# Optimization experiments

Measured on AMD Instinct MI355X. Metric: run time of the kernel, lower is better.

Reference implementation:

```python
import jax, jax.numpy as jnp
import numpy as np

WS = 8            # window size (square)
N = WS * WS       # tokens per window = 64
DIM = 192
HEADS = 6
HDIM = DIM // HEADS
SCALE = HDIM ** -0.5


def _rel_pos_index(ws=WS):
    coords = np.stack(np.meshgrid(np.arange(ws), np.arange(ws), indexing='ij'))  # [2,ws,ws]
    cf = coords.reshape(2, -1)                       # [2, N]
    rc = (cf[:, :, None] - cf[:, None, :]).transpose(1, 2, 0).astype(np.int64)  # [N,N,2]
    rc[:, :, 0] += ws - 1
    rc[:, :, 1] += ws - 1
    rc[:, :, 0] *= 2 * ws - 1
    return jnp.asarray(rc.sum(-1))                   # [N, N]

REL_IDX = _rel_pos_index()


def _linear(x, w, b=None):
    y = jnp.einsum('...i,oi->...o', x, w)
    return y if b is None else y + b


def _diff_attn(q_t, k_t, v_t, q_r, k_r, v_r, bias, lam):
    # q,k,v: [B, H, N, d]; bias: [H, N, N]; lam scalar
    at = jax.nn.softmax(jnp.einsum('bhqd,bhkd->bhqk', q_t * SCALE, k_t) + bias, axis=-1)
    ar = jax.nn.softmax(jnp.einsum('bhqd,bhkd->bhqk', q_r * SCALE, k_r) + bias, axis=-1)
    dt = at - lam * ar
    dr = ar - lam * at
    ot = jnp.einsum('bhqk,bhkd->bhqd', dt, v_t)
    orf = jnp.einsum('bhqk,bhkd->bhqd', dr, v_r)
    return ot, orf


def _heads(x, B):
    # [B, N, C] -> [B, H, N, d]
    return x.reshape(B, N, HEADS, HDIM).transpose(0, 2, 1, 3)


def _unheads(x, B):
    return x.transpose(0, 2, 1, 3).reshape(B, N, DIM)


def setup_inputs() -> dict:
    key = jax.random.key(0)
    ks = jax.random.split(key, 16)
    nW = 1024
    p = lambda k, shp: (jax.random.normal(k, shp, jnp.float32) * 0.02)
    return {
        'x_windows': jax.random.normal(ks[0], (nW, N, DIM), jnp.float32),
        'y_windows': jax.random.normal(ks[1], (nW, N, DIM), jnp.float32),
        'sa_qkv_w': p(ks[2], (3 * DIM, DIM)), 'sa_qkv_b': jnp.zeros((3 * DIM,), jnp.float32),
        'sa_ct_w': p(ks[3], (DIM, DIM)), 'sa_cr_w': p(ks[4], (DIM, DIM)),
        'ca_q_w': p(ks[5], (DIM, DIM)), 'ca_q_b': jnp.zeros((DIM,), jnp.float32),
        'ca_kv_w': p(ks[6], (2 * DIM, DIM)), 'ca_kv_b': jnp.zeros((2 * DIM,), jnp.float32),
        'ca_ct_w': p(ks[7], (DIM, DIM)), 'ca_cr_w': p(ks[8], (DIM, DIM)),
        'rpb_table': p(ks[9], ((2 * WS - 1) * (2 * WS - 1), HEADS)),
        'proj_sa_w': p(ks[10], (DIM, DIM)), 'proj_sa_b': jnp.zeros((DIM,), jnp.float32),
        'proj_ca_w': p(ks[11], (DIM, DIM)), 'proj_ca_b': jnp.zeros((DIM,), jnp.float32),
        'lambda_sa': jnp.float32(0.1), 'lambda_ca': jnp.float32(0.1),
        'sa_enh': jnp.float32(0.1), 'ca_enh': jnp.float32(0.1),
    }


def reference(x_windows, y_windows, sa_qkv_w, sa_qkv_b, sa_ct_w, sa_cr_w,
              ca_q_w, ca_q_b, ca_kv_w, ca_kv_b, ca_ct_w, ca_cr_w,
              rpb_table, proj_sa_w, proj_sa_b, proj_ca_w, proj_ca_b,
              lambda_sa, lambda_ca, sa_enh, ca_enh):
    B = x_windows.shape[0]
    bias = rpb_table[REL_IDX.reshape(-1)].reshape(N, N, HEADS).transpose(2, 0, 1)  # [H,N,N]

    # ---- Self-attention branch (batch-dim concat) ----
    t_enh = x_windows + sa_enh * _linear(y_windows, sa_cr_w)
    r_enh = y_windows + sa_enh * _linear(x_windows, sa_ct_w)
    qkv_t = _linear(t_enh, sa_qkv_w, sa_qkv_b).reshape(B, N, 3, HEADS, HDIM).transpose(2, 0, 3, 1, 4)
    qkv_r = _linear(r_enh, sa_qkv_w, sa_qkv_b).reshape(B, N, 3, HEADS, HDIM).transpose(2, 0, 3, 1, 4)
    lam_sa = jnp.clip(jax.nn.sigmoid(lambda_sa), 0.01, 0.99)
    ot, orf = _diff_attn(qkv_t[0], qkv_t[1], qkv_t[2], qkv_r[0], qkv_r[1], qkv_r[2], bias, lam_sa)
    sa_t = _linear(_unheads(ot, B), proj_sa_w, proj_sa_b)
    sa_r = _linear(_unheads(orf, B), proj_sa_w, proj_sa_b)
    sa_out = jnp.concatenate([sa_t, sa_r], axis=0)  # [2B, N, C]

    # ---- Cross-attention branch (seq-dim concat) ----
    t_enh = x_windows + ca_enh * _linear(y_windows, ca_cr_w)
    r_enh = y_windows + ca_enh * _linear(x_windows, ca_ct_w)
    q_t = _heads(_linear(t_enh, ca_q_w, ca_q_b), B)
    q_r = _heads(_linear(r_enh, ca_q_w, ca_q_b), B)
    xcat = jnp.concatenate([t_enh, r_enh], axis=1)  # [B, 2N, C]
    kv = _linear(xcat, ca_kv_w, ca_kv_b).reshape(B, 2 * N, 2, HEADS, HDIM).transpose(2, 0, 3, 1, 4)
    k, v = kv[0], kv[1]
    k_t, k_r = k[:, :, :N], k[:, :, N:]
    v_t, v_r = v[:, :, :N], v[:, :, N:]
    lam_ca = jnp.clip(jax.nn.sigmoid(lambda_ca), 0.01, 0.99)
    ot, orf = _diff_attn(q_t, k_t, v_t, q_r, k_r, v_r, bias, lam_ca)
    ca_t = _linear(_unheads(ot, B), proj_ca_w, proj_ca_b)
    ca_r = _linear(_unheads(orf, B), proj_ca_w, proj_ca_b)
    ca_out = jnp.concatenate([ca_t, ca_r], axis=1)  # [B, 2N, C]

    # pack into a single array: [4B, N, C]
    return jnp.concatenate([sa_out, ca_out.reshape(2 * B, N, DIM)], axis=0)
```

## Files before the change

kernel.cpp:

```cpp
#include <hip/hip_runtime.h>

#define KD 192
#define H6 6

typedef __attribute__((ext_vector_type(8))) short bf16x8;
typedef __attribute__((ext_vector_type(4))) float f32x4;

__device__ __forceinline__ unsigned short f2bf(float f) {
  unsigned u = __float_as_uint(f);
  u += 0x7FFFu + ((u >> 16) & 1u);
  return (unsigned short)(u >> 16);
}

__global__ void bias_k(const float* __restrict__ tab, float* __restrict__ biasw) {
  int t = blockIdx.x * 256 + threadIdx.x;
  if (t >= H6 * 64 * 64) return;
  int h = t >> 12, rem = t & 4095, i = rem >> 6, j = rem & 63;
  int idx = ((i >> 3) - (j >> 3) + 7) * 15 + ((i & 7) - (j & 7) + 7);
  biasw[t] = tab[idx * H6 + h];
}

__global__ void convert_k(
    const float* __restrict__ sa_qkv_w, const float* __restrict__ sa_ct_w,
    const float* __restrict__ sa_cr_w, const float* __restrict__ ca_q_w,
    const float* __restrict__ ca_kv_w, const float* __restrict__ ca_ct_w,
    const float* __restrict__ ca_cr_w, const float* __restrict__ proj_sa_w,
    const float* __restrict__ proj_ca_w,
    const float* __restrict__ ca_q_b, const float* __restrict__ ca_kv_b,
    unsigned short* __restrict__ wqkv, unsigned short* __restrict__ wct_sa,
    unsigned short* __restrict__ wcr_sa, unsigned short* __restrict__ wca,
    unsigned short* __restrict__ wct_ca, unsigned short* __restrict__ wcr_ca,
    unsigned short* __restrict__ wpsa, unsigned short* __restrict__ wpca,
    float* __restrict__ bca)
{
  int t = blockIdx.x * 256 + threadIdx.x;
  if (t < 110592) {
    int i = t << 2;
    const float* s; unsigned short* d;
    if (i < 110592)      { s = sa_qkv_w + i;            d = wqkv + i; }
    else if (i < 147456) { s = sa_ct_w + (i - 110592);  d = wct_sa + (i - 110592); }
    else if (i < 184320) { s = sa_cr_w + (i - 147456);  d = wcr_sa + (i - 147456); }
    else if (i < 221184) { s = ca_q_w + (i - 184320);   d = wca + (i - 184320); }
    else if (i < 294912) { s = ca_kv_w + (i - 221184);  d = wca + 36864 + (i - 221184); }
    else if (i < 331776) { s = ca_ct_w + (i - 294912);  d = wct_ca + (i - 294912); }
    else if (i < 368640) { s = ca_cr_w + (i - 331776);  d = wcr_ca + (i - 331776); }
    else if (i < 405504) { s = proj_sa_w + (i - 368640); d = wpsa + (i - 368640); }
    else                 { s = proj_ca_w + (i - 405504); d = wpca + (i - 405504); }
    float4 v = *(const float4*)s;
    ushort4 p;
    p.x = f2bf(v.x); p.y = f2bf(v.y); p.z = f2bf(v.z); p.w = f2bf(v.w);
    *(ushort4*)d = p;
  } else if (t < 110592 + 144) {
    int i = (t - 110592) << 2;
    const float* s = (i < 192) ? (ca_q_b + i) : (ca_kv_b + (i - 192));
    *(float4*)(bca + i) = *(const float4*)s;
  }
}

struct FQArgs {
  const unsigned short* Wc[4];
  const unsigned short* Wq[4];
  const float* bias[4];
  unsigned short* dq[4];
  unsigned short* dk[4];
  unsigned short* dv[4];
};

__global__ __launch_bounds__(256) void fqkv_k(
    const float* __restrict__ x, const float* __restrict__ y,
    const float* __restrict__ sap, const float* __restrict__ cap,
    FQArgs args, float SC)
{
  __shared__ short Al[64][200], Wl[64][200], El[64][200];
  const int tid = threadIdx.x;
  const int mblk = blockIdx.x, z = blockIdx.y;
  const int row = tid >> 2, cb = (tid & 3) * 48;
  const float* A    = (z & 1) ? x : y;
  const float* resd = (z & 1) ? y : x;
  const float sc = (z < 2) ? *sap : *cap;

  {
    const float* ap = A + ((long)mblk * 64 + row) * KD + cb;
#pragma unroll
    for (int j = 0; j < 12; ++j) {
      float4 v = *(const float4*)(ap + 4 * j);
      ushort4 p;
      p.x = f2bf(v.x); p.y = f2bf(v.y); p.z = f2bf(v.z); p.w = f2bf(v.w);
      *(ushort4*)&Al[row][cb + 4 * j] = p;
    }
  }
  const int lane = tid & 63, wv = tid >> 6;
  const int qn = lane & 15, g = lane >> 4;
  const int mloc = 16 * wv + 4 * g;
  const f32x4 zero = {0.f, 0.f, 0.f, 0.f};

  for (int ct = 0; ct < 3; ++ct) {
    {
      const unsigned short* Wp = args.Wc[z] + ((long)ct * 64 + row) * KD + cb;
#pragma unroll
      for (int j = 0; j < 6; ++j)
        *(float4*)&Wl[row][cb + 8 * j] = *(const float4*)(Wp + 8 * j);
    }
    __syncthreads();
    f32x4 acc[4];
#pragma unroll
    for (int nt = 0; nt < 4; ++nt) acc[nt] = zero;
#pragma unroll
    for (int ks = 0; ks < 6; ++ks) {
      bf16x8 a = *(const bf16x8*)&Al[16 * wv + qn][32 * ks + 8 * g];
#pragma unroll
      for (int nt = 0; nt < 4; ++nt) {
        bf16x8 bfr = *(const bf16x8*)&Wl[16 * nt + qn][32 * ks + 8 * g];
        acc[nt] = __builtin_amdgcn_mfma_f32_16x16x32_bf16(a, bfr, acc[nt], 0, 0, 0);
      }
    }
#pragma unroll
    for (int nt = 0; nt < 4; ++nt) {
      const int c = ct * 64 + 16 * nt + qn;
#pragma unroll
      for (int r = 0; r < 4; ++r)
        El[mloc + r][c] =
            f2bf(resd[((long)mblk * 64 + mloc + r) * KD + c] + sc * acc[nt][r]);
    }
    __syncthreads();
  }

  for (int wt = 0; wt < 9; ++wt) {
    {
      const unsigned short* Wp = args.Wq[z] + ((long)wt * 64 + row) * KD + cb;
#pragma unroll
      for (int j = 0; j < 6; ++j)
        *(float4*)&Wl[row][cb + 8 * j] = *(const float4*)(Wp + 8 * j);
    }
    __syncthreads();
    f32x4 acc[4];
#pragma unroll
    for (int nt = 0; nt < 4; ++nt) acc[nt] = zero;
#pragma unroll
    for (int ks = 0; ks < 6; ++ks) {
      bf16x8 a = *(const bf16x8*)&El[16 * wv + qn][32 * ks + 8 * g];
#pragma unroll
      for (int nt = 0; nt < 4; ++nt) {
        bf16x8 bfr = *(const bf16x8*)&Wl[16 * nt + qn][32 * ks + 8 * g];
        acc[nt] = __builtin_amdgcn_mfma_f32_16x16x32_bf16(a, bfr, acc[nt], 0, 0, 0);
      }
    }
#pragma unroll
    for (int nt = 0; nt < 4; ++nt) {
      const int cg = wt * 64 + 16 * nt + qn;
      const int idx = (cg >= 384) ? 2 : ((cg >= 192) ? 1 : 0);
      const int cc = cg - idx * KD;
      const int h = cc >> 5, d = cc & 31;
      const float bv = args.bias[z][cg];
      const float sca = (idx == 0) ? SC : 1.f;
      const long bwh = (long)mblk * H6 + h;
      if (idx < 2) {
        unsigned short* dst = idx ? args.dk[z] : args.dq[z];
#pragma unroll
        for (int r = 0; r < 4; ++r)
          dst[(bwh * 64 + (mloc + r)) * 32 + d] = f2bf((acc[nt][r] + bv) * sca);
      } else {
        ushort4 p;
        p.x = f2bf(acc[nt][0] + bv);
        p.y = f2bf(acc[nt][1] + bv);
        p.z = f2bf(acc[nt][2] + bv);
        p.w = f2bf(acc[nt][3] + bv);
        *(ushort4*)&args.dv[z][(bwh * 32 + d) * 64 + mloc] = p;
      }
    }
    __syncthreads();
  }
}

struct ProjArgs {
  const unsigned short* A[4];
  const unsigned short* W[4];
  const float* bias[4];
  float* o[4];
  long wstride[4];
};

__global__ __launch_bounds__(256) void proj_k(ProjArgs args)
{
  __shared__ short Al[64][200], Wl[64][200];
  const int tid = threadIdx.x;
  const int mblk = blockIdx.x, z = blockIdx.y;
  const int row = tid >> 2, cb = (tid & 3) * 48;
  {
    const unsigned short* A = args.A[z] + ((long)mblk * 64 + row) * KD + cb;
#pragma unroll
    for (int j = 0; j < 6; ++j)
      *(float4*)&Al[row][cb + 8 * j] = *(const float4*)(A + 8 * j);
  }
  const int lane = tid & 63, wv = tid >> 6;
  const int qn = lane & 15, g = lane >> 4;
  const int mloc = 16 * wv + 4 * g;
  const f32x4 zero = {0.f, 0.f, 0.f, 0.f};
  float* fo = args.o[z] + (long)mblk * args.wstride[z];

  for (int ct = 0; ct < 3; ++ct) {
    {
      const unsigned short* Wp = args.W[z] + ((long)ct * 64 + row) * KD + cb;
#pragma unroll
      for (int j = 0; j < 6; ++j)
        *(float4*)&Wl[row][cb + 8 * j] = *(const float4*)(Wp + 8 * j);
    }
    __syncthreads();
    f32x4 acc[4];
#pragma unroll
    for (int nt = 0; nt < 4; ++nt) acc[nt] = zero;
#pragma unroll
    for (int ks = 0; ks < 6; ++ks) {
      bf16x8 a = *(const bf16x8*)&Al[16 * wv + qn][32 * ks + 8 * g];
#pragma unroll
      for (int nt = 0; nt < 4; ++nt) {
        bf16x8 bfr = *(const bf16x8*)&Wl[16 * nt + qn][32 * ks + 8 * g];
        acc[nt] = __builtin_amdgcn_mfma_f32_16x16x32_bf16(a, bfr, acc[nt], 0, 0, 0);
      }
    }
#pragma unroll
    for (int nt = 0; nt < 4; ++nt) {
      const int c = ct * 64 + 16 * nt + qn;
      const float bv = args.bias[z][c];
#pragma unroll
      for (int r = 0; r < 4; ++r)
        fo[(long)(mloc + r) * KD + c] = acc[nt][r] + bv;
    }
    __syncthreads();
  }
}

__device__ __forceinline__ void softmax_rows2(f32x4 (&S)[4][2]) {
#pragma unroll
  for (int nt = 0; nt < 2; ++nt) {
    float mx = -3.0e38f;
#pragma unroll
    for (int mt = 0; mt < 4; ++mt)
#pragma unroll
      for (int r = 0; r < 4; ++r) mx = fmaxf(mx, S[mt][nt][r]);
    mx = fmaxf(mx, __shfl_xor(mx, 16));
    mx = fmaxf(mx, __shfl_xor(mx, 32));
    float sm = 0.f;
#pragma unroll
    for (int mt = 0; mt < 4; ++mt)
#pragma unroll
      for (int r = 0; r < 4; ++r) {
        float p = __expf(S[mt][nt][r] - mx);
        S[mt][nt][r] = p;
        sm += p;
      }
    sm += __shfl_xor(sm, 16);
    sm += __shfl_xor(sm, 32);
    const float inv = 1.f / sm;
#pragma unroll
    for (int mt = 0; mt < 4; ++mt)
#pragma unroll
      for (int r = 0; r < 4; ++r) S[mt][nt][r] *= inv;
  }
}

__device__ __forceinline__ void diff_attn32(
    const unsigned short* __restrict__ qb, const unsigned short* __restrict__ kb,
    const unsigned short* __restrict__ vTb, long pstride,
    const float* __restrict__ bh, float lam,
    unsigned short* __restrict__ o_t, unsigned short* __restrict__ o_r,
    long base, int b, int h, int qoff, int qn, int g,
    short (*Pl)[32][72])
{
  f32x4 st[4][2], sr[4][2];
#pragma unroll
  for (int mt = 0; mt < 4; ++mt)
#pragma unroll
    for (int nt = 0; nt < 2; ++nt) {
      f32x4 bv = *(const f32x4*)&bh[(qoff + 16 * nt + qn) * 64 + 16 * mt + 4 * g];
      st[mt][nt] = bv;
      sr[mt][nt] = bv;
    }
  {
    bf16x8 ka[4], qv[2];
#pragma unroll
    for (int mt = 0; mt < 4; ++mt)
      ka[mt] = *(const bf16x8*)&kb[base + (16 * mt + qn) * 32 + 8 * g];
#pragma unroll
    for (int nt = 0; nt < 2; ++nt)
      qv[nt] = *(const bf16x8*)&qb[base + (qoff + 16 * nt + qn) * 32 + 8 * g];
#pragma unroll
    for (int mt = 0; mt < 4; ++mt)
#pragma unroll
      for (int nt = 0; nt < 2; ++nt)
        st[mt][nt] = __builtin_amdgcn_mfma_f32_16x16x32_bf16(ka[mt], qv[nt], st[mt][nt], 0, 0, 0);
#pragma unroll
    for (int mt = 0; mt < 4; ++mt)
      ka[mt] = *(const bf16x8*)&kb[pstride + base + (16 * mt + qn) * 32 + 8 * g];
#pragma unroll
    for (int nt = 0; nt < 2; ++nt)
      qv[nt] = *(const bf16x8*)&qb[pstride + base + (qoff + 16 * nt + qn) * 32 + 8 * g];
#pragma unroll
    for (int mt = 0; mt < 4; ++mt)
#pragma unroll
      for (int nt = 0; nt < 2; ++nt)
        sr[mt][nt] = __builtin_amdgcn_mfma_f32_16x16x32_bf16(ka[mt], qv[nt], sr[mt][nt], 0, 0, 0);
  }
  softmax_rows2(st);
  softmax_rows2(sr);
#pragma unroll
  for (int mt = 0; mt < 4; ++mt)
#pragma unroll
    for (int nt = 0; nt < 2; ++nt) {
      ushort4 pt, pr;
#pragma unroll
      for (int r = 0; r < 4; ++r) {
        float a = st[mt][nt][r], rr = sr[mt][nt][r];
        ((unsigned short*)&pt)[r] = f2bf(a - lam * rr);
        ((unsigned short*)&pr)[r] = f2bf(rr - lam * a);
      }
      *(ushort4*)&Pl[0][16 * nt + qn][16 * mt + 4 * g] = pt;
      *(ushort4*)&Pl[1][16 * nt + qn][16 * mt + 4 * g] = pr;
    }
  const f32x4 zero = {0.f, 0.f, 0.f, 0.f};
#pragma unroll
  for (int p = 0; p < 2; ++p) {
    const unsigned short* vv = p ? (vTb + pstride) : vTb;
    unsigned short* outp = p ? o_r : o_t;
    f32x4 oa[2][2];
#pragma unroll
    for (int i = 0; i < 2; ++i)
#pragma unroll
      for (int nt = 0; nt < 2; ++nt) oa[i][nt] = zero;
#pragma unroll
    for (int ks = 0; ks < 2; ++ks) {
      bf16x8 va0 = *(const bf16x8*)&vv[base + (0 + qn) * 64 + 32 * ks + 8 * g];
      bf16x8 va1 = *(const bf16x8*)&vv[base + (16 + qn) * 64 + 32 * ks + 8 * g];
#pragma unroll
      for (int nt = 0; nt < 2; ++nt) {
        bf16x8 pb = *(const bf16x8*)&Pl[p][16 * nt + qn][32 * ks + 8 * g];
        oa[0][nt] = __builtin_amdgcn_mfma_f32_16x16x32_bf16(va0, pb, oa[0][nt], 0, 0, 0);
        oa[1][nt] = __builtin_amdgcn_mfma_f32_16x16x32_bf16(va1, pb, oa[1][nt], 0, 0, 0);
      }
    }
#pragma unroll
    for (int d16 = 0; d16 < 2; ++d16)
#pragma unroll
      for (int nt = 0; nt < 2; ++nt) {
        const int q = qoff + 16 * nt + qn;
        ushort4 pk;
        pk.x = f2bf(oa[d16][nt][0]); pk.y = f2bf(oa[d16][nt][1]);
        pk.z = f2bf(oa[d16][nt][2]); pk.w = f2bf(oa[d16][nt][3]);
        *(ushort4*)&outp[((long)b * 64 + q) * KD + h * 32 + 16 * d16 + 4 * g] = pk;
      }
  }
}

__global__ __launch_bounds__(256) void attn_k(
    const unsigned short* __restrict__ saq, const unsigned short* __restrict__ sak,
    const unsigned short* __restrict__ savT,
    const unsigned short* __restrict__ caq, const unsigned short* __restrict__ cak,
    const unsigned short* __restrict__ cavT,
    const float* __restrict__ biasw, const float* __restrict__ lsp,
    const float* __restrict__ lcp,
    unsigned short* __restrict__ o0, unsigned short* __restrict__ o1,
    unsigned short* __restrict__ o2, unsigned short* __restrict__ o3,
    long pstride)
{
  __shared__ short Pl[4][2][32][72];
  const int wv = threadIdx.x >> 6, lane = threadIdx.x & 63;
  const int qn = lane & 15, g = lane >> 4;
  const int qoff = (wv & 1) * 32;
  const int wh = blockIdx.x * 2 + (wv >> 1);
  const int b = wh / H6, h = wh - b * H6;
  const float* bh = biasw + (long)h * 4096;
  const long base = (long)wh * 2048;
  float ls = 1.f / (1.f + __expf(-*lsp));
  ls = fminf(fmaxf(ls, 0.01f), 0.99f);
  float lc = 1.f / (1.f + __expf(-*lcp));
  lc = fminf(fmaxf(lc, 0.01f), 0.99f);
  diff_attn32(saq, sak, savT, pstride, bh, ls, o0, o1, base, b, h, qoff, qn, g, Pl[wv]);
  diff_attn32(caq, cak, cavT, pstride, bh, lc, o2, o3, base, b, h, qoff, qn, g, Pl[wv]);
}

extern "C" void kernel_launch(void* const* d_in, const int* in_sizes, int n_in,
                              void* d_out, int out_size, void* d_ws, size_t ws_size,
                              hipStream_t stream)
{
  const float* x         = (const float*)d_in[0];
  const float* y         = (const float*)d_in[1];
  const float* sa_qkv_w  = (const float*)d_in[2];
  const float* sa_qkv_b  = (const float*)d_in[3];
  const float* sa_ct_w   = (const float*)d_in[4];
  const float* sa_cr_w   = (const float*)d_in[5];
  const float* ca_q_w    = (const float*)d_in[6];
  const float* ca_q_b    = (const float*)d_in[7];
  const float* ca_kv_w   = (const float*)d_in[8];
  const float* ca_kv_b   = (const float*)d_in[9];
  const float* ca_ct_w   = (const float*)d_in[10];
  const float* ca_cr_w   = (const float*)d_in[11];
  const float* rpb       = (const float*)d_in[12];
  const float* proj_sa_w = (const float*)d_in[13];
  const float* proj_sa_b = (const float*)d_in[14];
  const float* proj_ca_w = (const float*)d_in[15];
  const float* proj_ca_b = (const float*)d_in[16];
  const float* lam_sa_p  = (const float*)d_in[17];
  const float* lam_ca_p  = (const float*)d_in[18];
  const float* sa_enh_p  = (const float*)d_in[19];
  const float* ca_enh_p  = (const float*)d_in[20];
  float* out = (float*)d_out;

  const int M = in_sizes[0] / KD;
  const int B = M / 64;
  const long pstride = (long)B * H6 * 2048;

  char* ws = (char*)d_ws;
  float* biasw = (float*)ws;
  float* bca = (float*)(ws + 98304);
  unsigned short* wqkv   = (unsigned short*)(ws + 100864);
  unsigned short* wca    = (unsigned short*)(ws + 322048);
  unsigned short* wct_sa = (unsigned short*)(ws + 543232);
  unsigned short* wcr_sa = (unsigned short*)(ws + 616960);
  unsigned short* wct_ca = (unsigned short*)(ws + 690688);
  unsigned short* wcr_ca = (unsigned short*)(ws + 764416);
  unsigned short* wpsa   = (unsigned short*)(ws + 838144);
  unsigned short* wpca   = (unsigned short*)(ws + 911872);
  long off = 1048576;
  unsigned short* ob0 = (unsigned short*)(ws + off); off += (long)M * KD * 2;
  unsigned short* ob1 = (unsigned short*)(ws + off); off += (long)M * KD * 2;
  unsigned short* ob2 = (unsigned short*)(ws + off); off += (long)M * KD * 2;
  unsigned short* ob3 = (unsigned short*)(ws + off); off += (long)M * KD * 2;
  unsigned short* caq  = (unsigned short*)(ws + off); off += pstride * 4;
  unsigned short* cak  = (unsigned short*)(ws + off); off += pstride * 4;
  unsigned short* cavT = (unsigned short*)(ws + off); off += pstride * 4;
  unsigned short* saq  = (unsigned short*)d_out;
  unsigned short* sak  = saq + 2 * pstride;
  unsigned short* savT = sak + 2 * pstride;

  const float SC = 0.17677669529663687f;

  convert_k<<<dim3(433), dim3(256), 0, stream>>>(
      sa_qkv_w, sa_ct_w, sa_cr_w, ca_q_w, ca_kv_w, ca_ct_w, ca_cr_w,
      proj_sa_w, proj_ca_w, ca_q_b, ca_kv_b,
      wqkv, wct_sa, wcr_sa, wca, wct_ca, wcr_ca, wpsa, wpca, bca);
  bias_k<<<dim3(96), dim3(256), 0, stream>>>(rpb, biasw);

  FQArgs fa;
  fa.Wc[0] = wcr_sa; fa.Wc[1] = wct_sa; fa.Wc[2] = wcr_ca; fa.Wc[3] = wct_ca;
  fa.Wq[0] = wqkv;   fa.Wq[1] = wqkv;   fa.Wq[2] = wca;    fa.Wq[3] = wca;
  fa.bias[0] = sa_qkv_b; fa.bias[1] = sa_qkv_b; fa.bias[2] = bca; fa.bias[3] = bca;
  fa.dq[0] = saq;  fa.dq[1] = saq + pstride;  fa.dq[2] = caq;  fa.dq[3] = caq + pstride;
  fa.dk[0] = sak;  fa.dk[1] = sak + pstride;  fa.dk[2] = cak;  fa.dk[3] = cak + pstride;
  fa.dv[0] = savT; fa.dv[1] = savT + pstride; fa.dv[2] = cavT; fa.dv[3] = cavT + pstride;
  fqkv_k<<<dim3(B, 4), dim3(256), 0, stream>>>(x, y, sa_enh_p, ca_enh_p, fa, SC);

  attn_k<<<dim3(B * H6 / 2), dim3(256), 0, stream>>>(saq, sak, savT, caq, cak, cavT,
                                                     biasw, lam_sa_p, lam_ca_p,
                                                     ob0, ob1, ob2, ob3, pstride);

  ProjArgs pa;
  pa.A[0] = ob0; pa.A[1] = ob1; pa.A[2] = ob2; pa.A[3] = ob3;
  pa.W[0] = wpsa; pa.W[1] = wpsa; pa.W[2] = wpca; pa.W[3] = wpca;
  pa.bias[0] = proj_sa_b; pa.bias[1] = proj_sa_b; pa.bias[2] = proj_ca_b; pa.bias[3] = proj_ca_b;
  pa.o[0] = out;                       pa.wstride[0] = 12288;
  pa.o[1] = out + (long)B * 12288;     pa.wstride[1] = 12288;
  pa.o[2] = out + (long)2 * B * 12288; pa.wstride[2] = 24576;
  pa.o[3] = out + (long)2 * B * 12288 + 12288; pa.wstride[3] = 24576;
  proj_k<<<dim3(B, 4), dim3(256), 0, stream>>>(pa);
}
```

Measured before the change: 665.6 us.

## Restructure fused QKV kernel with register prefetch, 2x2 warp tiling, shared A/E buffer

The fused cross-enhance + QKV projection kernel now prefetches the next 64-row weight tile into registers while MFMAs run on the current tile, so global loads overlap with compute. Warps switch from 16x64 strips to 32x32 quadrant tiles, with A fragments held in registers and reused across weight tiles, which cuts LDS reads. The input and enhanced-activation buffers are merged into one shared array so LDS use drops, and launch bounds request 3 blocks per CU. The cost is higher register pressure from the prefetch registers, A fragments and three sets of accumulators, which could limit occupancy or cause spills.

```diff
diff --git a/kernel.cpp b/kernel.cpp
--- a/kernel.cpp
+++ b/kernel.cpp
@@ -66,12 +66,13 @@
   unsigned short* dv[4];
 };
 
-__global__ __launch_bounds__(256) void fqkv_k(
+__global__ __launch_bounds__(256, 3) void fqkv_k(
     const float* __restrict__ x, const float* __restrict__ y,
     const float* __restrict__ sap, const float* __restrict__ cap,
     FQArgs args, float SC)
 {
-  __shared__ short Al[64][200], Wl[64][200], El[64][200];
+  __shared__ short AE[64][200];
+  __shared__ short Wl[64][200];
   const int tid = threadIdx.x;
   const int mblk = blockIdx.x, z = blockIdx.y;
   const int row = tid >> 2, cb = (tid & 3) * 48;
@@ -79,96 +80,136 @@
   const float* resd = (z & 1) ? y : x;
   const float sc = (z < 2) ? *sap : *cap;
 
+  float4 wpf[6];
   {
     const float* ap = A + ((long)mblk * 64 + row) * KD + cb;
+    const unsigned short* wp = args.Wc[z] + (long)row * KD + cb;
+#pragma unroll
+    for (int j = 0; j < 6; ++j) wpf[j] = *(const float4*)(wp + 8 * j);
 #pragma unroll
     for (int j = 0; j < 12; ++j) {
       float4 v = *(const float4*)(ap + 4 * j);
       ushort4 p;
       p.x = f2bf(v.x); p.y = f2bf(v.y); p.z = f2bf(v.z); p.w = f2bf(v.w);
-      *(ushort4*)&Al[row][cb + 4 * j] = p;
-    }
-  }
+      *(ushort4*)&AE[row][cb + 4 * j] = p;
+    }
+#pragma unroll
+    for (int j = 0; j < 6; ++j) *(float4*)&Wl[row][cb + 8 * j] = wpf[j];
+  }
+  __syncthreads();
+
   const int lane = tid & 63, wv = tid >> 6;
   const int qn = lane & 15, g = lane >> 4;
-  const int mloc = 16 * wv + 4 * g;
+  const int rbase = (wv & 1) * 32, cbase = (wv >> 1) * 32;
   const f32x4 zero = {0.f, 0.f, 0.f, 0.f};
 
-  for (int ct = 0; ct < 3; ++ct) {
+  bf16x8 af[2][6];
+#pragma unroll
+  for (int im = 0; im < 2; ++im)
+#pragma unroll
+    for (int ks = 0; ks < 6; ++ks)
+      af[im][ks] = *(const bf16x8*)&AE[rbase + 16 * im + qn][32 * ks + 8 * g];
+
+  f32x4 acc2[3][2][2];
+#pragma unroll
+  for (int t = 0; t < 3; ++t)
+#pragma unroll
+    for (int im = 0; im < 2; ++im)
+#pragma unroll
+      for (int in = 0; in < 2; ++in) acc2[t][im][in] = zero;
+
+#pragma unroll
+  for (int t = 0; t < 3; ++t) {
     {
-      const unsigned short* Wp = args.Wc[z] + ((long)ct * 64 + row) * KD + cb;
-#pragma unroll
-      for (int j = 0; j < 6; ++j)
-        *(float4*)&Wl[row][cb + 8 * j] = *(const float4*)(Wp + 8 * j);
+      const unsigned short* ns = (t < 2) ? (args.Wc[z] + (long)(t + 1) * 12288)
+                                         : args.Wq[z];
+      const unsigned short* wp = ns + (long)row * KD + cb;
+#pragma unroll
+      for (int j = 0; j < 6; ++j) wpf[j] = *(const float4*)(wp + 8 * j);
+    }
+#pragma unroll
+    for (int ks = 0; ks < 6; ++ks) {
+      bf16x8 wf0 = *(const bf16x8*)&Wl[cbase + qn][32 * ks + 8 * g];
+      bf16x8 wf1 = *(const bf16x8*)&Wl[cbase + 16 + qn][32 * ks + 8 * g];
+      acc2[t][0][0] = __builtin_amdgcn_mfma_f32_16x16x32_bf16(af[0][ks], wf0, acc2[t][0][0], 0, 0, 0);
+      acc2[t][1][0] = __builtin_amdgcn_mfma_f32_16x16x32_bf16(af[1][ks], wf0, acc2[t][1][0], 0, 0, 0);
+      acc2[t][0][1] = __builtin_amdgcn_mfma_f32_16x16x32_bf16(af[0][ks], wf1, acc2[t][0][1], 0, 0, 0);
+      acc2[t][1][1] = __builtin_amdgcn_mfma_f32_16x16x32_bf16(af[1][ks], wf1, acc2[t][1][1], 0, 0, 0);
     }
     __syncthreads();
-    f32x4 acc[4];
-#pragma unroll
-    for (int nt = 0; nt < 4; ++nt) acc[nt] = zero;
+#pragma unroll
+    for (int j = 0; j < 6; ++j) *(float4*)&Wl[row][cb + 8 * j] = wpf[j];
+    __syncthreads();
+  }
+
+#pragma unroll
+  for (int ct = 0; ct < 3; ++ct)
+#pragma unroll
+    for (int im = 0; im < 2; ++im)
+#pragma unroll
+      for (int in = 0; in < 2; ++in) {
+        const int c = ct * 64 + cbase + 16 * in + qn;
+        const int rl = rbase + 16 * im + 4 * g;
+#pragma unroll
+        for (int r = 0; r < 4; ++r)
+          AE[rl + r][c] = f2bf(resd[((long)mblk * 64 + rl + r) * KD + c] +
+                               sc * acc2[ct][im][in][r]);
+      }
+  __syncthreads();
+#pragma unroll
+  for (int im = 0; im < 2; ++im)
+#pragma unroll
+    for (int ks = 0; ks < 6; ++ks)
+      af[im][ks] = *(const bf16x8*)&AE[rbase + 16 * im + qn][32 * ks + 8 * g];
+
+  for (int wt = 0; wt < 9; ++wt) {
+    if (wt < 8) {
+      const unsigned short* wp = args.Wq[z] + (long)(wt + 1) * 12288 + (long)row * KD + cb;
+#pragma unroll
+      for (int j = 0; j < 6; ++j) wpf[j] = *(const float4*)(wp + 8 * j);
+    }
+    f32x4 acc[2][2] = {{zero, zero}, {zero, zero}};
 #pragma unroll
     for (int ks = 0; ks < 6; ++ks) {
-      bf16x8 a = *(const bf16x8*)&Al[16 * wv + qn][32 * ks + 8 * g];
-#pragma unroll
-      for (int nt = 0; nt < 4; ++nt) {
-        bf16x8 bfr = *(const bf16x8*)&Wl[16 * nt + qn][32 * ks + 8 * g];
-        acc[nt] = __builtin_amdgcn_mfma_f32_16x16x32_bf16(a, bfr, acc[nt], 0, 0, 0);
-      }
-    }
-#pragma unroll
-    for (int nt = 0; nt < 4; ++nt) {
-      const int c = ct * 64 + 16 * nt + qn;
-#pragma unroll
-      for (int r = 0; r < 4; ++r)
-        El[mloc + r][c] =
-            f2bf(resd[((long)mblk * 64 + mloc + r) * KD + c] + sc * acc[nt][r]);
-    }
-    __syncthreads();
-  }
-
-  for (int wt = 0; wt < 9; ++wt) {
-    {
-      const unsigned short* Wp = args.Wq[z] + ((long)wt * 64 + row) * KD + cb;
-#pragma unroll
-      for (int j = 0; j < 6; ++j)
-        *(float4*)&Wl[row][cb + 8 * j] = *(const float4*)(Wp + 8 * j);
-    }
-    __syncthreads();
-    f32x4 acc[4];
-#pragma unroll
-    for (int nt = 0; nt < 4; ++nt) acc[nt] = zero;
-#pragma unroll
-    for (int ks = 0; ks < 6; ++ks) {
-      bf16x8 a = *(const bf16x8*)&El[16 * wv + qn][32 * ks + 8 * g];
-#pragma unroll
-      for (int nt = 0; nt < 4; ++nt) {
-        bf16x8 bfr = *(const bf16x8*)&Wl[16 * nt + qn][32 * ks + 8 * g];
-        acc[nt] = __builtin_amdgcn_mfma_f32_16x16x32_bf16(a, bfr, acc[nt], 0, 0, 0);
-      }
-    }
-#pragma unroll
-    for (int nt = 0; nt < 4; ++nt) {
-      const int cg = wt * 64 + 16 * nt + qn;
-      const int idx = (cg >= 384) ? 2 : ((cg >= 192) ? 1 : 0);
-      const int cc = cg - idx * KD;
-      const int h = cc >> 5, d = cc & 31;
-      const float bv = args.bias[z][cg];
-      const float sca = (idx == 0) ? SC : 1.f;
-      const long bwh = (long)mblk * H6 + h;
-      if (idx < 2) {
-        unsigned short* dst = idx ? args.dk[z] : args.dq[z];
-#pragma unroll
-        for (int r = 0; r < 4; ++r)
-          dst[(bwh * 64 + (mloc + r)) * 32 + d] = f2bf((acc[nt][r] + bv) * sca);
-      } else {
-        ushort4 p;
-        p.x = f2bf(acc[nt][0] + bv);
-        p.y = f2bf(acc[nt][1] + bv);
-        p.z = f2bf(acc[nt][2] + bv);
-        p.w = f2bf(acc[nt][3] + bv);
-        *(ushort4*)&args.dv[z][(bwh * 32 + d) * 64 + mloc] = p;
-      }
-    }
-    __syncthreads();
+      bf16x8 wf0 = *(const bf16x8*)&Wl[cbase + qn][32 * ks + 8 * g];
+      bf16x8 wf1 = *(const bf16x8*)&Wl[cbase + 16 + qn][32 * ks + 8 * g];
+      acc[0][0] = __builtin_amdgcn_mfma_f32_16x16x32_bf16(af[0][ks], wf0, acc[0][0], 0, 0, 0);
+      acc[1][0] = __builtin_amdgcn_mfma_f32_16x16x32_bf16(af[1][ks], wf0, acc[1][0], 0, 0, 0);
+      acc[0][1] = __builtin_amdgcn_mfma_f32_16x16x32_bf16(af[0][ks], wf1, acc[0][1], 0, 0, 0);
+      acc[1][1] = __builtin_amdgcn_mfma_f32_16x16x32_bf16(af[1][ks], wf1, acc[1][1], 0, 0, 0);
+    }
+#pragma unroll
+    for (int im = 0; im < 2; ++im)
+#pragma unroll
+      for (int in = 0; in < 2; ++in) {
+        const int cg = wt * 64 + cbase + 16 * in + qn;
+        const int idx = (cg >= 384) ? 2 : ((cg >= 192) ? 1 : 0);
+        const int cc = cg - idx * KD;
+        const int h = cc >> 5, d = cc & 31;
+        const float bv = args.bias[z][cg];
+        const long bwh = (long)mblk * H6 + h;
+        const int rl = rbase + 16 * im + 4 * g;
+        if (idx < 2) {
+          const float sca = idx ? 1.f : SC;
+          unsigned short* dst = idx ? args.dk[z] : args.dq[z];
+#pragma unroll
+          for (int r = 0; r < 4; ++r)
+            dst[(bwh * 64 + rl + r) * 32 + d] = f2bf((acc[im][in][r] + bv) * sca);
+        } else {
+          ushort4 p;
+          p.x = f2bf(acc[im][in][0] + bv);
+          p.y = f2bf(acc[im][in][1] + bv);
+          p.z = f2bf(acc[im][in][2] + bv);
+          p.w = f2bf(acc[im][in][3] + bv);
+          *(ushort4*)&args.dv[z][(bwh * 32 + d) * 64 + rl] = p;
+        }
+      }
+    if (wt < 8) {
+      __syncthreads();
+#pragma unroll
+      for (int j = 0; j < 6; ++j) *(float4*)&Wl[row][cb + 8 * j] = wpf[j];
+      __syncthreads();
+    }
   }
 }
 
```

New measurement: 865.0 us. 29.9% more time.

## Fuse differential attention with output projection in one per-window kernel

Applied to the files above, without the earlier changes.

Adds a fattn_k kernel with one block per window and branch, using 12 waves (one per head and query half). Each block computes both differential attention outputs into shared memory as bf16, then applies the output projection with bias straight into the final buffer. This removes the attention output round trip through global memory and one kernel launch. It needs a larger workspace to hold all q/k/v tensors, so the old three-kernel path is kept as a fallback when the workspace is too small. The 768-thread blocks use a lot of LDS, which may limit occupancy.

```diff
diff --git a/kernel.cpp b/kernel.cpp
--- a/kernel.cpp
+++ b/kernel.cpp
@@ -172,64 +172,6 @@
   }
 }
 
-struct ProjArgs {
-  const unsigned short* A[4];
-  const unsigned short* W[4];
-  const float* bias[4];
-  float* o[4];
-  long wstride[4];
-};
-
-__global__ __launch_bounds__(256) void proj_k(ProjArgs args)
-{
-  __shared__ short Al[64][200], Wl[64][200];
-  const int tid = threadIdx.x;
-  const int mblk = blockIdx.x, z = blockIdx.y;
-  const int row = tid >> 2, cb = (tid & 3) * 48;
-  {
-    const unsigned short* A = args.A[z] + ((long)mblk * 64 + row) * KD + cb;
-#pragma unroll
-    for (int j = 0; j < 6; ++j)
-      *(float4*)&Al[row][cb + 8 * j] = *(const float4*)(A + 8 * j);
-  }
-  const int lane = tid & 63, wv = tid >> 6;
-  const int qn = lane & 15, g = lane >> 4;
-  const int mloc = 16 * wv + 4 * g;
-  const f32x4 zero = {0.f, 0.f, 0.f, 0.f};
-  float* fo = args.o[z] + (long)mblk * args.wstride[z];
-
-  for (int ct = 0; ct < 3; ++ct) {
-    {
-      const unsigned short* Wp = args.W[z] + ((long)ct * 64 + row) * KD + cb;
-#pragma unroll
-      for (int j = 0; j < 6; ++j)
-        *(float4*)&Wl[row][cb + 8 * j] = *(const float4*)(Wp + 8 * j);
-    }
-    __syncthreads();
-    f32x4 acc[4];
-#pragma unroll
-    for (int nt = 0; nt < 4; ++nt) acc[nt] = zero;
-#pragma unroll
-    for (int ks = 0; ks < 6; ++ks) {
-      bf16x8 a = *(const bf16x8*)&Al[16 * wv + qn][32 * ks + 8 * g];
-#pragma unroll
-      for (int nt = 0; nt < 4; ++nt) {
-        bf16x8 bfr = *(const bf16x8*)&Wl[16 * nt + qn][32 * ks + 8 * g];
-        acc[nt] = __builtin_amdgcn_mfma_f32_16x16x32_bf16(a, bfr, acc[nt], 0, 0, 0);
-      }
-    }
-#pragma unroll
-    for (int nt = 0; nt < 4; ++nt) {
-      const int c = ct * 64 + 16 * nt + qn;
-      const float bv = args.bias[z][c];
-#pragma unroll
-      for (int r = 0; r < 4; ++r)
-        fo[(long)(mloc + r) * KD + c] = acc[nt][r] + bv;
-    }
-    __syncthreads();
-  }
-}
-
 __device__ __forceinline__ void softmax_rows2(f32x4 (&S)[4][2]) {
 #pragma unroll
   for (int nt = 0; nt < 2; ++nt) {
@@ -256,6 +198,157 @@
     for (int mt = 0; mt < 4; ++mt)
 #pragma unroll
       for (int r = 0; r < 4; ++r) S[mt][nt][r] *= inv;
+  }
+}
+
+struct FAArgs {
+  const unsigned short* q[2];
+  const unsigned short* k[2];
+  const unsigned short* vT[2];
+  const float* lamp[2];
+  const unsigned short* w[2];
+  const float* pb[2];
+  float* ot[2];
+  float* orr[2];
+  long ostride[2];
+};
+
+__global__ __launch_bounds__(768, 3) void fattn_k(
+    FAArgs args, const float* __restrict__ biasw, long pstride)
+{
+  __shared__ short Ol[2][64][200];
+  __shared__ short Pl[12][32][72];
+  const int tid = threadIdx.x;
+  const int wv = tid >> 6, lane = tid & 63;
+  const int qn = lane & 15, g = lane >> 4;
+  const int b = blockIdx.x, z = blockIdx.y;
+  const int h = wv >> 1, qoff = (wv & 1) * 32;
+  const long base = ((long)b * H6 + h) * 2048;
+  const unsigned short* qb = args.q[z];
+  const unsigned short* kb = args.k[z];
+  const unsigned short* vTb = args.vT[z];
+  float lam = 1.f / (1.f + __expf(-*args.lamp[z]));
+  lam = fminf(fmaxf(lam, 0.01f), 0.99f);
+  const float* bh = biasw + (long)h * 4096;
+  short (*pl)[72] = Pl[wv];
+  const f32x4 zero = {0.f, 0.f, 0.f, 0.f};
+
+  f32x4 st[4][2], sr[4][2];
+#pragma unroll
+  for (int mt = 0; mt < 4; ++mt)
+#pragma unroll
+    for (int nt = 0; nt < 2; ++nt) {
+      f32x4 bv = *(const f32x4*)&bh[(qoff + 16 * nt + qn) * 64 + 16 * mt + 4 * g];
+      st[mt][nt] = bv;
+      sr[mt][nt] = bv;
+    }
+  {
+    bf16x8 ka[4], qv[2];
+#pragma unroll
+    for (int mt = 0; mt < 4; ++mt)
+      ka[mt] = *(const bf16x8*)&kb[base + (16 * mt + qn) * 32 + 8 * g];
+#pragma unroll
+    for (int nt = 0; nt < 2; ++nt)
+      qv[nt] = *(const bf16x8*)&qb[base + (qoff + 16 * nt + qn) * 32 + 8 * g];
+#pragma unroll
+    for (int mt = 0; mt < 4; ++mt)
+#pragma unroll
+      for (int nt = 0; nt < 2; ++nt)
+        st[mt][nt] = __builtin_amdgcn_mfma_f32_16x16x32_bf16(ka[mt], qv[nt], st[mt][nt], 0, 0, 0);
+#pragma unroll
+    for (int mt = 0; mt < 4; ++mt)
+      ka[mt] = *(const bf16x8*)&kb[pstride + base + (16 * mt + qn) * 32 + 8 * g];
+#pragma unroll
+    for (int nt = 0; nt < 2; ++nt)
+      qv[nt] = *(const bf16x8*)&qb[pstride + base + (qoff + 16 * nt + qn) * 32 + 8 * g];
+#pragma unroll
+    for (int mt = 0; mt < 4; ++mt)
+#pragma unroll
+      for (int nt = 0; nt < 2; ++nt)
+        sr[mt][nt] = __builtin_amdgcn_mfma_f32_16x16x32_bf16(ka[mt], qv[nt], sr[mt][nt], 0, 0, 0);
+  }
+  softmax_rows2(st);
+  softmax_rows2(sr);
+#pragma unroll
+  for (int mt = 0; mt < 4; ++mt)
+#pragma unroll
+    for (int nt = 0; nt < 2; ++nt)
+#pragma unroll
+      for (int r = 0; r < 4; ++r) {
+        float a = st[mt][nt][r], rr = sr[mt][nt][r];
+        st[mt][nt][r] = a - lam * rr;
+        sr[mt][nt][r] = rr - lam * a;
+      }
+
+#pragma unroll
+  for (int p = 0; p < 2; ++p) {
+    auto& P = p ? sr : st;
+#pragma unroll
+    for (int mt = 0; mt < 4; ++mt)
+#pragma unroll
+      for (int nt = 0; nt < 2; ++nt) {
+        ushort4 pk;
+        pk.x = f2bf(P[mt][nt][0]); pk.y = f2bf(P[mt][nt][1]);
+        pk.z = f2bf(P[mt][nt][2]); pk.w = f2bf(P[mt][nt][3]);
+        *(ushort4*)&pl[16 * nt + qn][16 * mt + 4 * g] = pk;
+      }
+    const unsigned short* vv = p ? (vTb + pstride) : vTb;
+    f32x4 oa[2][2];
+#pragma unroll
+    for (int i = 0; i < 2; ++i)
+#pragma unroll
+      for (int nt = 0; nt < 2; ++nt) oa[i][nt] = zero;
+#pragma unroll
+    for (int ks = 0; ks < 2; ++ks) {
+      bf16x8 va0 = *(const bf16x8*)&vv[base + (0 + qn) * 64 + 32 * ks + 8 * g];
+      bf16x8 va1 = *(const bf16x8*)&vv[base + (16 + qn) * 64 + 32 * ks + 8 * g];
+#pragma unroll
+      for (int nt = 0; nt < 2; ++nt) {
+        bf16x8 pb8 = *(const bf16x8*)&pl[16 * nt + qn][32 * ks + 8 * g];
+        oa[0][nt] = __builtin_amdgcn_mfma_f32_16x16x32_bf16(va0, pb8, oa[0][nt], 0, 0, 0);
+        oa[1][nt] = __builtin_amdgcn_mfma_f32_16x16x32_bf16(va1, pb8, oa[1][nt], 0, 0, 0);
+      }
+    }
+#pragma unroll
+    for (int d16 = 0; d16 < 2; ++d16)
+#pragma unroll
+      for (int nt = 0; nt < 2; ++nt) {
+        ushort4 pk;
+        pk.x = f2bf(oa[d16][nt][0]); pk.y = f2bf(oa[d16][nt][1]);
+        pk.z = f2bf(oa[d16][nt][2]); pk.w = f2bf(oa[d16][nt][3]);
+        *(ushort4*)&Ol[p][qoff + 16 * nt + qn][h * 32 + 16 * d16 + 4 * g] = pk;
+      }
+  }
+
+  const int cstrip = wv * 16;
+  const unsigned short* wz = args.w[z];
+  bf16x8 wf[6];
+#pragma unroll
+  for (int ks = 0; ks < 6; ++ks)
+    wf[ks] = *(const bf16x8*)&wz[(long)(cstrip + qn) * KD + 32 * ks + 8 * g];
+  f32x4 biasv = *(const f32x4*)&args.pb[z][cstrip + 4 * g];
+  __syncthreads();
+
+#pragma unroll
+  for (int p = 0; p < 2; ++p) {
+    f32x4 acc[4];
+#pragma unroll
+    for (int mt = 0; mt < 4; ++mt) acc[mt] = zero;
+#pragma unroll
+    for (int ks = 0; ks < 6; ++ks)
+#pragma unroll
+      for (int mt = 0; mt < 4; ++mt) {
+        bf16x8 of = *(const bf16x8*)&Ol[p][16 * mt + qn][32 * ks + 8 * g];
+        acc[mt] = __builtin_amdgcn_mfma_f32_16x16x32_bf16(wf[ks], of, acc[mt], 0, 0, 0);
+      }
+    float* fo = (p ? args.orr[z] : args.ot[z]) + (long)b * args.ostride[z];
+#pragma unroll
+    for (int mt = 0; mt < 4; ++mt) {
+      f32x4 res;
+#pragma unroll
+      for (int r = 0; r < 4; ++r) res[r] = acc[mt][r] + biasv[r];
+      *(f32x4*)&fo[(long)(16 * mt + qn) * KD + cstrip + 4 * g] = res;
+    }
   }
 }
 
@@ -376,6 +469,64 @@
   lc = fminf(fmaxf(lc, 0.01f), 0.99f);
   diff_attn32(saq, sak, savT, pstride, bh, ls, o0, o1, base, b, h, qoff, qn, g, Pl[wv]);
   diff_attn32(caq, cak, cavT, pstride, bh, lc, o2, o3, base, b, h, qoff, qn, g, Pl[wv]);
+}
+
+struct ProjArgs {
+  const unsigned short* A[4];
+  const unsigned short* W[4];
+  const float* bias[4];
+  float* o[4];
+  long wstride[4];
+};
+
+__global__ __launch_bounds__(256) void proj_k(ProjArgs args)
+{
+  __shared__ short Al[64][200], Wl[64][200];
+  const int tid = threadIdx.x;
+  const int mblk = blockIdx.x, z = blockIdx.y;
+  const int row = tid >> 2, cb = (tid & 3) * 48;
+  {
+    const unsigned short* A = args.A[z] + ((long)mblk * 64 + row) * KD + cb;
+#pragma unroll
+    for (int j = 0; j < 6; ++j)
+      *(float4*)&Al[row][cb + 8 * j] = *(const float4*)(A + 8 * j);
+  }
+  const int lane = tid & 63, wv = tid >> 6;
+  const int qn = lane & 15, g = lane >> 4;
+  const int mloc = 16 * wv + 4 * g;
+  const f32x4 zero = {0.f, 0.f, 0.f, 0.f};
+  float* fo = args.o[z] + (long)mblk * args.wstride[z];
+
+  for (int ct = 0; ct < 3; ++ct) {
+    {
+      const unsigned short* Wp = args.W[z] + ((long)ct * 64 + row) * KD + cb;
+#pragma unroll
+      for (int j = 0; j < 6; ++j)
+        *(float4*)&Wl[row][cb + 8 * j] = *(const float4*)(Wp + 8 * j);
+    }
+    __syncthreads();
+    f32x4 acc[4];
+#pragma unroll
+    for (int nt = 0; nt < 4; ++nt) acc[nt] = zero;
+#pragma unroll
+    for (int ks = 0; ks < 6; ++ks) {
+      bf16x8 a = *(const bf16x8*)&Al[16 * wv + qn][32 * ks + 8 * g];
+#pragma unroll
+      for (int nt = 0; nt < 4; ++nt) {
+        bf16x8 bfr = *(const bf16x8*)&Wl[16 * nt + qn][32 * ks + 8 * g];
+        acc[nt] = __builtin_amdgcn_mfma_f32_16x16x32_bf16(a, bfr, acc[nt], 0, 0, 0);
+      }
+    }
+#pragma unroll
+    for (int nt = 0; nt < 4; ++nt) {
+      const int c = ct * 64 + 16 * nt + qn;
+      const float bv = args.bias[z][c];
+#pragma unroll
+      for (int r = 0; r < 4; ++r)
+        fo[(long)(mloc + r) * KD + c] = acc[nt][r] + bv;
+    }
+    __syncthreads();
+  }
 }
 
 extern "C" void kernel_launch(void* const* d_in, const int* in_sizes, int n_in,
@@ -420,17 +571,10 @@
   unsigned short* wcr_ca = (unsigned short*)(ws + 764416);
   unsigned short* wpsa   = (unsigned short*)(ws + 838144);
   unsigned short* wpca   = (unsigned short*)(ws + 911872);
-  long off = 1048576;
-  unsigned short* ob0 = (unsigned short*)(ws + off); off += (long)M * KD * 2;
-  unsigned short* ob1 = (unsigned short*)(ws + off); off += (long)M * KD * 2;
-  unsigned short* ob2 = (unsigned short*)(ws + off); off += (long)M * KD * 2;
-  unsigned short* ob3 = (unsigned short*)(ws + off); off += (long)M * KD * 2;
-  unsigned short* caq  = (unsigned short*)(ws + off); off += pstride * 4;
-  unsigned short* cak  = (unsigned short*)(ws + off); off += pstride * 4;
-  unsigned short* cavT = (unsigned short*)(ws + off); off += pstride * 4;
-  unsigned short* saq  = (unsigned short*)d_out;
-  unsigned short* sak  = saq + 2 * pstride;
-  unsigned short* savT = sak + 2 * pstride;
+
+  const size_t TEN = (size_t)pstride * 4;
+  const size_t NEED = 1048576 + 6 * TEN;
+  const bool fused = (ws_size >= NEED);
 
   const float SC = 0.17677669529663687f;
 
@@ -440,26 +584,72 @@
       wqkv, wct_sa, wcr_sa, wca, wct_ca, wcr_ca, wpsa, wpca, bca);
   bias_k<<<dim3(96), dim3(256), 0, stream>>>(rpb, biasw);
 
-  FQArgs fa;
-  fa.Wc[0] = wcr_sa; fa.Wc[1] = wct_sa; fa.Wc[2] = wcr_ca; fa.Wc[3] = wct_ca;
-  fa.Wq[0] = wqkv;   fa.Wq[1] = wqkv;   fa.Wq[2] = wca;    fa.Wq[3] = wca;
-  fa.bias[0] = sa_qkv_b; fa.bias[1] = sa_qkv_b; fa.bias[2] = bca; fa.bias[3] = bca;
-  fa.dq[0] = saq;  fa.dq[1] = saq + pstride;  fa.dq[2] = caq;  fa.dq[3] = caq + pstride;
-  fa.dk[0] = sak;  fa.dk[1] = sak + pstride;  fa.dk[2] = cak;  fa.dk[3] = cak + pstride;
-  fa.dv[0] = savT; fa.dv[1] = savT + pstride; fa.dv[2] = cavT; fa.dv[3] = cavT + pstride;
-  fqkv_k<<<dim3(B, 4), dim3(256), 0, stream>>>(x, y, sa_enh_p, ca_enh_p, fa, SC);
-
-  attn_k<<<dim3(B * H6 / 2), dim3(256), 0, stream>>>(saq, sak, savT, caq, cak, cavT,
-                                                     biasw, lam_sa_p, lam_ca_p,
-                                                     ob0, ob1, ob2, ob3, pstride);
-
-  ProjArgs pa;
-  pa.A[0] = ob0; pa.A[1] = ob1; pa.A[2] = ob2; pa.A[3] = ob3;
-  pa.W[0] = wpsa; pa.W[1] = wpsa; pa.W[2] = wpca; pa.W[3] = wpca;
-  pa.bias[0] = proj_sa_b; pa.bias[1] = proj_sa_b; pa.bias[2] = proj_ca_b; pa.bias[3] = proj_ca_b;
-  pa.o[0] = out;                       pa.wstride[0] = 12288;
-  pa.o[1] = out + (long)B * 12288;     pa.wstride[1] = 12288;
-  pa.o[2] = out + (long)2 * B * 12288; pa.wstride[2] = 24576;
-  pa.o[3] = out + (long)2 * B * 12288 + 12288; pa.wstride[3] = 24576;
-  proj_k<<<dim3(B, 4), dim3(256), 0, stream>>>(pa);
-}
+  if (fused) {
+    long off = 1048576;
+    unsigned short* saq  = (unsigned short*)(ws + off); off += TEN;
+    unsigned short* sak  = (unsigned short*)(ws + off); off += TEN;
+    unsigned short* savT = (unsigned short*)(ws + off); off += TEN;
+    unsigned short* caq  = (unsigned short*)(ws + off); off += TEN;
+    unsigned short* cak  = (unsigned short*)(ws + off); off += TEN;
+    unsigned short* cavT = (unsigned short*)(ws + off);
+
+    FQArgs fa;
+    fa.Wc[0] = wcr_sa; fa.Wc[1] = wct_sa; fa.Wc[2] = wcr_ca; fa.Wc[3] = wct_ca;
+    fa.Wq[0] = wqkv;   fa.Wq[1] = wqkv;   fa.Wq[2] = wca;    fa.Wq[3] = wca;
+    fa.bias[0] = sa_qkv_b; fa.bias[1] = sa_qkv_b; fa.bias[2] = bca; fa.bias[3] = bca;
+    fa.dq[0] = saq;  fa.dq[1] = saq + pstride;  fa.dq[2] = caq;  fa.dq[3] = caq + pstride;
+    fa.dk[0] = sak;  fa.dk[1] = sak + pstride;  fa.dk[2] = cak;  fa.dk[3] = cak + pstride;
+    fa.dv[0] = savT; fa.dv[1] = savT + pstride; fa.dv[2] = cavT; fa.dv[3] = cavT + pstride;
+    fqkv_k<<<dim3(B, 4), dim3(256), 0, stream>>>(x, y, sa_enh_p, ca_enh_p, fa, SC);
+
+    FAArgs aa;
+    aa.q[0] = saq;  aa.q[1] = caq;
+    aa.k[0] = sak;  aa.k[1] = cak;
+    aa.vT[0] = savT; aa.vT[1] = cavT;
+    aa.lamp[0] = lam_sa_p; aa.lamp[1] = lam_ca_p;
+    aa.w[0] = wpsa; aa.w[1] = wpca;
+    aa.pb[0] = proj_sa_b; aa.pb[1] = proj_ca_b;
+    aa.ot[0]  = out;
+    aa.orr[0] = out + (long)B * 12288;
+    aa.ot[1]  = out + (long)2 * B * 12288;
+    aa.orr[1] = out + (long)2 * B * 12288 + 12288;
+    aa.ostride[0] = 12288;
+    aa.ostride[1] = 24576;
+    fattn_k<<<dim3(B, 2), dim3(768), 0, stream>>>(aa, biasw, pstride);
+  } else {
+    long off = 1048576;
+    unsigned short* ob0 = (unsigned short*)(ws + off); off += (long)M * KD * 2;
+    unsigned short* ob1 = (unsigned short*)(ws + off); off += (long)M * KD * 2;
+    unsigned short* ob2 = (unsigned short*)(ws + off); off += (long)M * KD * 2;
+    unsigned short* ob3 = (unsigned short*)(ws + off); off += (long)M * KD * 2;
+    unsigned short* caq  = (unsigned short*)(ws + off); off += TEN;
+    unsigned short* cak  = (unsigned short*)(ws + off); off += TEN;
+    unsigned short* cavT = (unsigned short*)(ws + off);
+    unsigned short* saq  = (unsigned short*)d_out;
+    unsigned short* sak  = saq + 2 * pstride;
+    unsigned short* savT = sak + 2 * pstride;
+
+    FQArgs fa;
+    fa.Wc[0] = wcr_sa; fa.Wc[1] = wct_sa; fa.Wc[2] = wcr_ca; fa.Wc[3] = wct_ca;
+    fa.Wq[0] = wqkv;   fa.Wq[1] = wqkv;   fa.Wq[2] = wca;    fa.Wq[3] = wca;
+    fa.bias[0] = sa_qkv_b; fa.bias[1] = sa_qkv_b; fa.bias[2] = bca; fa.bias[3] = bca;
+    fa.dq[0] = saq;  fa.dq[1] = saq + pstride;  fa.dq[2] = caq;  fa.dq[3] = caq + pstride;
+    fa.dk[0] = sak;  fa.dk[1] = sak + pstride;  fa.dk[2] = cak;  fa.dk[3] = cak + pstride;
+    fa.dv[0] = savT; fa.dv[1] = savT + pstride; fa.dv[2] = cavT; fa.dv[3] = cavT + pstride;
+    fqkv_k<<<dim3(B, 4), dim3(256), 0, stream>>>(x, y, sa_enh_p, ca_enh_p, fa, SC);
+
+    attn_k<<<dim3(B * H6 / 2), dim3(256), 0, stream>>>(saq, sak, savT, caq, cak, cavT,
+                                                       biasw, lam_sa_p, lam_ca_p,
+                                                       ob0, ob1, ob2, ob3, pstride);
+
+    ProjArgs pa;
+    pa.A[0] = ob0; pa.A[1] = ob1; pa.A[2] = ob2; pa.A[3] = ob3;
+    pa.W[0] = wpsa; pa.W[1] = wpsa; pa.W[2] = wpca; pa.W[3] = wpca;
+    pa.bias[0] = proj_sa_b; pa.bias[1] = proj_sa_b; pa.bias[2] = proj_ca_b; pa.bias[3] = proj_ca_b;
+    pa.o[0] = out;                       pa.wstride[0] = 12288;
+    pa.o[1] = out + (long)B * 12288;     pa.wstride[1] = 12288;
+    pa.o[2] = out + (long)2 * B * 12288; pa.wstride[2] = 24576;
+    pa.o[3] = out + (long)2 * B * 12288 + 12288; pa.wstride[3] = 24576;
+    proj_k<<<dim3(B, 4), dim3(256), 0, stream>>>(pa);
+  }
+}
```

New measurement: 636.4 us. 4.4% less time.
